# Kernel optimization log

Measured on AMD Instinct MI355X. Metric: run time of the kernel, lower is better.

The kernel has to match this reference:

```python
import jax, jax.numpy as jnp
import numpy as np

B, T, V = 4, 2048, 2048
D = 256   # state_dim
R = 512   # inner_dim
EPS = float(jnp.finfo(jnp.float32).eps)  # F.rms_norm default eps = dtype eps


def rms_norm(x):
    return x * jax.lax.rsqrt(jnp.mean(x * x, axis=-1, keepdims=True) + EPS)


def setup_inputs() -> dict:
    key = jax.random.key(0)
    ks = jax.random.split(key, 9)
    std = 0.02
    return {
        "x": jax.random.normal(ks[0], (B, T, V), dtype=jnp.float32),
        "Wq": jax.random.normal(ks[1], (D, V), dtype=jnp.float32) * std,
        "Wk": jax.random.normal(ks[2], (D, V), dtype=jnp.float32) * std,
        "Wv": jax.random.normal(ks[3], (D, V), dtype=jnp.float32) * std,
        "Wo": jax.random.normal(ks[4], (V, D), dtype=jnp.float32) * std,
        "decay_logit": jnp.float32(3.0),
        "q_out_scale": jnp.float32(0.1),
        "Wdown": jax.random.normal(ks[5], (R, V), dtype=jnp.float32) * std,
        "Wup": jax.random.normal(ks[6], (V, R), dtype=jnp.float32) * std,
        "t_bias": jnp.zeros((R,), dtype=jnp.float32),
        "t_out_scale": jnp.float32(0.1),
        "q_scale": jnp.ones((1,), dtype=jnp.float32),
        "t_scale": jnp.ones((1,), dtype=jnp.float32),
    }


def qtable(x, Wq, Wk, Wv, Wo, decay_logit, out_scale):
    # x: (B,T,V)
    q = jnp.einsum('btv,dv->btd', x, Wq)
    k = jnp.einsum('btv,dv->btd', x, Wk)
    v = jnp.einsum('btv,dv->btd', x, Wv)
    scores = jnp.einsum('btd,bsd->bts', q, k)  # (B,T,T)
    decay = jax.nn.sigmoid(decay_logit)
    pos = jnp.arange(T)
    diff = pos[None, :] - pos[:, None]  # diff[t,s] = s - t ... matches torch (unsqueeze(0)-unsqueeze(1))
    causal = (diff > 0).astype(jnp.float32)
    weights = decay ** jnp.clip(diff.astype(jnp.float32) - 1.0, 0.0, None) * causal
    scores = scores * weights[None, :, :]
    retrieved = jnp.einsum('bts,bsd->btd', scores, v)
    return jnp.einsum('btd,vd->btv', retrieved, Wo) * out_scale


def transform(x, Wdown, Wup, bias, out_scale):
    h = jnp.einsum('btv,rv->btr', x, Wdown) + bias
    h = jax.nn.gelu(h, approximate=False)
    return jnp.einsum('btr,vr->btv', h, Wup) * out_scale


def reference(x, Wq, Wk, Wv, Wo, decay_logit, q_out_scale,
              Wdown, Wup, t_bias, t_out_scale, q_scale, t_scale):
    x = x + q_scale * qtable(rms_norm(x), Wq, Wk, Wv, Wo, decay_logit, q_out_scale)
    x = x + t_scale * transform(rms_norm(x), Wdown, Wup, t_bias, t_out_scale)
    return x
```

## Files before the change

### kernel.cpp

```cpp
#include <hip/hip_runtime.h>
#include <cmath>

typedef _Float16 f16;
typedef _Float16 f16x8 __attribute__((ext_vector_type(8)));
typedef _Float16 f16x4 __attribute__((ext_vector_type(4)));
typedef float f32x4 __attribute__((ext_vector_type(4)));

#define MFMA16(a, b, c) __builtin_amdgcn_mfma_f32_16x16x32_f16(a, b, c, 0, 0, 0)

static constexpr int Bsz = 4;
static constexpr int T = 2048;
static constexpr int V = 2048;
static constexpr int D = 256;
static constexpr int R = 512;
static constexpr int M = Bsz * T;

__device__ __forceinline__ void load_lds16(const f16* g, f16* l) {
    __builtin_amdgcn_global_load_lds(
        (const __attribute__((address_space(1))) unsigned int*)(unsigned long long)g,
        (__attribute__((address_space(3))) unsigned int*)(unsigned int)(unsigned long long)l,
        16, 0, 0);
}

__global__ __launch_bounds__(256) void conv_all(const float* __restrict__ s0,
                                                const float* __restrict__ s1,
                                                const float* __restrict__ s2,
                                                const float* __restrict__ s3,
                                                const float* __restrict__ s4,
                                                const float* __restrict__ s5,
                                                f16* __restrict__ dst) {
    int idx = (blockIdx.x * 256 + threadIdx.x) * 4;
    if (idx >= 4194304) return;
    const float* src; int off;
    if      (idx <  524288) { src = s0; off = idx; }
    else if (idx < 1048576) { src = s1; off = idx - 524288; }
    else if (idx < 1572864) { src = s2; off = idx - 1048576; }
    else if (idx < 2097152) { src = s3; off = idx - 1572864; }
    else if (idx < 3145728) { src = s4; off = idx - 2097152; }
    else                    { src = s5; off = idx - 3145728; }
    float4 v = *(const float4*)&src[off];
    f16x4 o;
    o[0] = (f16)v.x; o[1] = (f16)v.y; o[2] = (f16)v.z; o[3] = (f16)v.w;
    *(f16x4*)&dst[idx] = o;
}

__global__ __launch_bounds__(256) void rmsnorm_kernel(const float* __restrict__ x,
                                                      f16* __restrict__ out) {
    int row = blockIdx.x;
    const float* xr = x + (size_t)row * V;
    int tid = threadIdx.x;
    float4 v0 = ((const float4*)xr)[tid];
    float4 v1 = ((const float4*)xr)[tid + 256];
    float ss = v0.x * v0.x + v0.y * v0.y + v0.z * v0.z + v0.w * v0.w
             + v1.x * v1.x + v1.y * v1.y + v1.z * v1.z + v1.w * v1.w;
    #pragma unroll
    for (int o = 32; o > 0; o >>= 1) ss += __shfl_xor(ss, o);
    __shared__ float wsum[4];
    if ((tid & 63) == 0) wsum[tid >> 6] = ss;
    __syncthreads();
    float tot = wsum[0] + wsum[1] + wsum[2] + wsum[3];
    float s = rsqrtf(tot / (float)V + 1.1920929e-07f);
    f16* orow = out + (size_t)row * V;
    f16x4 o0, o1;
    o0[0] = (f16)(v0.x * s); o0[1] = (f16)(v0.y * s);
    o0[2] = (f16)(v0.z * s); o0[3] = (f16)(v0.w * s);
    o1[0] = (f16)(v1.x * s); o1[1] = (f16)(v1.y * s);
    o1[2] = (f16)(v1.z * s); o1[3] = (f16)(v1.w * s);
    *(f16x4*)&orow[tid * 4] = o0;
    *(f16x4*)&orow[1024 + tid * 4] = o1;
}

__global__ __launch_bounds__(256) void rmsnorm_f16(const f16* __restrict__ x,
                                                   f16* __restrict__ out) {
    int row = blockIdx.x;
    int tid = threadIdx.x;
    const f16* xr = x + (size_t)row * V;
    f16x8 v = *(const f16x8*)&xr[tid * 8];
    float f[8];
    float ss = 0.f;
    #pragma unroll
    for (int j = 0; j < 8; j++) { f[j] = (float)v[j]; ss += f[j] * f[j]; }
    #pragma unroll
    for (int o = 32; o > 0; o >>= 1) ss += __shfl_xor(ss, o);
    __shared__ float wsum[4];
    if ((tid & 63) == 0) wsum[tid >> 6] = ss;
    __syncthreads();
    float tot = wsum[0] + wsum[1] + wsum[2] + wsum[3];
    float s = rsqrtf(tot / (float)V + 1.1920929e-07f);
    f16x8 o;
    #pragma unroll
    for (int j = 0; j < 8; j++) o[j] = (f16)(f[j] * s);
    *(f16x8*)&out[(size_t)row * V + tid * 8] = o;
}

struct GemmEpi {
    const float* residf;
    const f16* residh;
    float* outf;
    f16* outh;
    f16* out_q; f16* out_k; f16* out_vT;
    f16* out_h;
    const float* bias;
    const float* sA; const float* sB;
};

template <int MODE>
__device__ __forceinline__ void epi_store(const GemmEpi& e, float s, f32x4 a,
                                          int gm_base, int gn) {
    #pragma unroll
    for (int i = 0; i < 4; i++) {
        int gm = gm_base + i;
        float vv = a[i];
        if (MODE == 0) {
            if (gn < 256) {
                e.out_q[(size_t)gm * D + gn] = (f16)vv;
            } else if (gn < 512) {
                e.out_k[(size_t)gm * D + (gn - 256)] = (f16)vv;
            } else {
                int d = gn - 512;
                int b = gm >> 11, t = gm & 2047;
                e.out_vT[((size_t)b * D + d) * T + t] = (f16)vv;
            }
        } else if (MODE == 1) {
            size_t o = (size_t)gm * V + gn;
            e.outh[o] = (f16)(e.residf[o] + s * vv);
        } else if (MODE == 2) {
            float z = vv + e.bias[gn];
            float g = 0.5f * z * (1.f + erff(z * 0.70710678118654752f));
            e.out_h[(size_t)gm * R + gn] = (f16)g;
        } else {
            size_t o = (size_t)gm * V + gn;
            e.outf[o] = (float)e.residh[o] + s * vv;
        }
    }
}

template <int MODE>
__global__ __launch_bounds__(256) void gemm_nt(const f16* __restrict__ A,
                                               const f16* __restrict__ Bm,
                                               int K, GemmEpi e) {
    __shared__ f16 Asl[2][128 * 32];
    __shared__ f16 Bsl[2][128 * 32];
    int tid = threadIdx.x;
    int lane = tid & 63, wv = tid >> 6;
    int wm = wv >> 1, wn = wv & 1;
    int quad = lane >> 4, l16 = lane & 15;
    int m0 = blockIdx.x * 128, n0 = blockIdx.y * 128;
    f32x4 acc[4][4] = {};

    int srow = lane >> 2;
    int scg = (lane & 3) ^ ((lane >> 3) & 3);
    const f16* Ag0 = &A[(size_t)(m0 + 16 * wv + srow) * K + scg * 8];
    const f16* Ag1 = &A[(size_t)(m0 + 16 * (wv + 4) + srow) * K + scg * 8];
    const f16* Bg0 = &Bm[(size_t)(n0 + 16 * wv + srow) * K + scg * 8];
    const f16* Bg1 = &Bm[(size_t)(n0 + 16 * (wv + 4) + srow) * K + scg * 8];
    int lo0 = (16 * wv) * 32, lo1 = (16 * (wv + 4)) * 32;

    int fs = quad ^ ((l16 >> 1) & 3);
    int niter = K >> 5;

    load_lds16(Ag0, &Asl[0][lo0]);
    load_lds16(Ag1, &Asl[0][lo1]);
    load_lds16(Bg0, &Bsl[0][lo0]);
    load_lds16(Bg1, &Bsl[0][lo1]);

    for (int i = 0; i < niter; i++) {
        int cur = i & 1;
        __builtin_amdgcn_s_barrier();
        if (i + 1 < niter) {
            int k0 = (i + 1) << 5;
            int nb = cur ^ 1;
            load_lds16(Ag0 + k0, &Asl[nb][lo0]);
            load_lds16(Ag1 + k0, &Asl[nb][lo1]);
            load_lds16(Bg0 + k0, &Bsl[nb][lo0]);
            load_lds16(Bg1 + k0, &Bsl[nb][lo1]);
            asm volatile("s_waitcnt vmcnt(4)" ::: "memory");
        } else {
            asm volatile("s_waitcnt vmcnt(0)" ::: "memory");
        }
        __builtin_amdgcn_s_barrier();
        f16x8 af[4], bf[4];
        #pragma unroll
        for (int j = 0; j < 4; j++)
            af[j] = *(const f16x8*)&Asl[cur][(64 * wm + 16 * j + l16) * 32 + fs * 8];
        #pragma unroll
        for (int j = 0; j < 4; j++)
            bf[j] = *(const f16x8*)&Bsl[cur][(64 * wn + 16 * j + l16) * 32 + fs * 8];
        #pragma unroll
        for (int mi = 0; mi < 4; mi++)
            #pragma unroll
            for (int ni = 0; ni < 4; ni++)
                acc[mi][ni] = MFMA16(af[mi], bf[ni], acc[mi][ni]);
    }

    float s = 0.f;
    if (MODE == 1 || MODE == 3) s = e.sA[0] * e.sB[0];
    #pragma unroll
    for (int mi = 0; mi < 4; mi++)
        #pragma unroll
        for (int ni = 0; ni < 4; ni++)
            epi_store<MODE>(e, s, acc[mi][ni],
                            m0 + 64 * wm + 16 * mi + quad * 4,
                            n0 + 64 * wn + 16 * ni + l16);
}

template <int MODE>
__global__ __launch_bounds__(256) void gemm_nt_k64(const f16* __restrict__ A,
                                                   const f16* __restrict__ Bm,
                                                   int K, GemmEpi e) {
    __shared__ f16 Asl[2][128 * 64];
    __shared__ f16 Bsl[2][128 * 64];
    int tid = threadIdx.x;
    int lane = tid & 63, wv = tid >> 6;
    int wm = wv >> 1, wn = wv & 1;
    int quad = lane >> 4, l16 = lane & 15;
    int m0 = blockIdx.x * 128, n0 = blockIdx.y * 128;
    f32x4 acc[4][4] = {};

    int r8 = lane >> 3;
    int gcol = (lane & 7) ^ r8;
    const f16* Ag[4]; const f16* Bg[4]; int lo[4];
    #pragma unroll
    for (int j = 0; j < 4; j++) {
        int rbase = 8 * (wv + 4 * j);
        Ag[j] = &A[(size_t)(m0 + rbase + r8) * K + gcol * 8];
        Bg[j] = &Bm[(size_t)(n0 + rbase + r8) * K + gcol * 8];
        lo[j] = rbase * 64;
    }
    int niter = K >> 6;

    #pragma unroll
    for (int j = 0; j < 4; j++) {
        load_lds16(Ag[j], &Asl[0][lo[j]]);
        load_lds16(Bg[j], &Bsl[0][lo[j]]);
    }

    for (int i = 0; i < niter; i++) {
        int cur = i & 1;
        __builtin_amdgcn_s_barrier();
        if (i + 1 < niter) {
            int k0 = (i + 1) << 6;
            int nb = cur ^ 1;
            #pragma unroll
            for (int j = 0; j < 4; j++) {
                load_lds16(Ag[j] + k0, &Asl[nb][lo[j]]);
                load_lds16(Bg[j] + k0, &Bsl[nb][lo[j]]);
            }
            asm volatile("s_waitcnt vmcnt(8)" ::: "memory");
        } else {
            asm volatile("s_waitcnt vmcnt(0)" ::: "memory");
        }
        __builtin_amdgcn_s_barrier();
        #pragma unroll
        for (int kk = 0; kk < 2; kk++) {
            f16x8 af[4], bf[4];
            #pragma unroll
            for (int j = 0; j < 4; j++) {
                int row = 64 * wm + 16 * j + l16;
                int sl = (kk * 4 + quad) ^ (l16 & 7);
                af[j] = *(const f16x8*)&Asl[cur][row * 64 + sl * 8];
            }
            #pragma unroll
            for (int j = 0; j < 4; j++) {
                int row = 64 * wn + 16 * j + l16;
                int sl = (kk * 4 + quad) ^ (l16 & 7);
                bf[j] = *(const f16x8*)&Bsl[cur][row * 64 + sl * 8];
            }
            #pragma unroll
            for (int mi = 0; mi < 4; mi++)
                #pragma unroll
                for (int ni = 0; ni < 4; ni++)
                    acc[mi][ni] = MFMA16(af[mi], bf[ni], acc[mi][ni]);
        }
    }

    float s = 0.f;
    if (MODE == 1 || MODE == 3) s = e.sA[0] * e.sB[0];
    #pragma unroll
    for (int mi = 0; mi < 4; mi++)
        #pragma unroll
        for (int ni = 0; ni < 4; ni++)
            epi_store<MODE>(e, s, acc[mi][ni],
                            m0 + 64 * wm + 16 * mi + quad * 4,
                            n0 + 64 * wn + 16 * ni + l16);
}

__global__ __launch_bounds__(256) void attn_kernel(const f16* __restrict__ q,
                                                   const f16* __restrict__ k,
                                                   const f16* __restrict__ vT,
                                                   f16* __restrict__ ret,
                                                   const float* __restrict__ decay_logit) {
    __shared__ f16 Psl[32 * 72];
    int tid = threadIdx.x, lane = tid & 63, wv = tid >> 6;
    int quad = lane >> 4, l16 = lane & 15;
    int b = blockIdx.y, t0 = blockIdx.x * 32;
    const f16* qb = q + (size_t)b * T * D;
    const f16* kb = k + (size_t)b * T * D;
    const f16* vb = vT + (size_t)b * D * T;
    f16* rb = ret + (size_t)b * T * D;

    float dl = decay_logit[0];
    float decay = 1.f / (1.f + expf(-dl));
    float l2d = log2f(decay);
    float nl2d = -l2d;

    f16x8 qf[2][8];
    #pragma unroll
    for (int mi = 0; mi < 2; mi++)
        #pragma unroll
        for (int kk = 0; kk < 8; kk++)
            qf[mi][kk] = *(const f16x8*)&qb[(size_t)(t0 + 16 * mi + l16) * D + kk * 32 + quad * 8];

    f32x4 acc2[2][4] = {};

    for (int s0 = t0; s0 < T; s0 += 64) {
        if ((float)(s0 - t0 - 32) * nl2d > 25.f) break;
        int srow = s0 + 16 * wv + l16;
        int srcl = srow < T ? srow : T - 1;
        f32x4 sacc[2] = {};
        #pragma unroll
        for (int kk = 0; kk < 8; kk++) {
            f16x8 bf = *(const f16x8*)&kb[(size_t)srcl * D + kk * 32 + quad * 8];
            sacc[0] = MFMA16(qf[0][kk], bf, sacc[0]);
            sacc[1] = MFMA16(qf[1][kk], bf, sacc[1]);
        }
        __syncthreads();
        #pragma unroll
        for (int mi = 0; mi < 2; mi++) {
            #pragma unroll
            for (int i = 0; i < 4; i++) {
                int t_ = t0 + 16 * mi + quad * 4 + i;
                int diff = srow - t_;
                float w = (diff > 0 && srow < T) ? exp2f((float)(diff - 1) * l2d) : 0.f;
                Psl[(16 * mi + quad * 4 + i) * 72 + 16 * wv + l16] = (f16)(sacc[mi][i] * w);
            }
        }
        __syncthreads();
        #pragma unroll
        for (int kk = 0; kk < 2; kk++) {
            int sb = s0 + kk * 32 + quad * 8;
            if (sb >= T) sb = T - 8;
            f16x8 pa[2], vf[4];
            #pragma unroll
            for (int mi = 0; mi < 2; mi++)
                pa[mi] = *(const f16x8*)&Psl[(16 * mi + l16) * 72 + kk * 32 + quad * 8];
            #pragma unroll
            for (int ni = 0; ni < 4; ni++)
                vf[ni] = *(const f16x8*)&vb[(size_t)(64 * wv + 16 * ni + l16) * T + sb];
            #pragma unroll
            for (int mi = 0; mi < 2; mi++)
                #pragma unroll
                for (int ni = 0; ni < 4; ni++)
                    acc2[mi][ni] = MFMA16(pa[mi], vf[ni], acc2[mi][ni]);
        }
    }

    #pragma unroll
    for (int mi = 0; mi < 2; mi++) {
        #pragma unroll
        for (int ni = 0; ni < 4; ni++) {
            int t_ = t0 + 16 * mi + quad * 4;
            int d_ = 64 * wv + 16 * ni + l16;
            #pragma unroll
            for (int i = 0; i < 4; i++)
                rb[(size_t)(t_ + i) * D + d_] = (f16)acc2[mi][ni][i];
        }
    }
}

extern "C" void kernel_launch(void* const* d_in, const int* in_sizes, int n_in,
                              void* d_out, int out_size, void* d_ws, size_t ws_size,
                              hipStream_t stream) {
    const float* x           = (const float*)d_in[0];
    const float* Wq          = (const float*)d_in[1];
    const float* Wk          = (const float*)d_in[2];
    const float* Wv          = (const float*)d_in[3];
    const float* Wo          = (const float*)d_in[4];
    const float* decay_logit = (const float*)d_in[5];
    const float* q_out_scale = (const float*)d_in[6];
    const float* Wdown       = (const float*)d_in[7];
    const float* Wup         = (const float*)d_in[8];
    const float* t_bias      = (const float*)d_in[9];
    const float* t_out_scale = (const float*)d_in[10];
    const float* q_scale     = (const float*)d_in[11];
    const float* t_scale     = (const float*)d_in[12];

    char* ws = (char*)d_ws;
    f16* Wqkv16  = (f16*)ws;  ws += (size_t)768 * V * 2;
    f16* Wo16    = (f16*)ws;  ws += (size_t)V * D * 2;
    f16* Wdown16 = (f16*)ws;  ws += (size_t)R * V * 2;
    f16* Wup16   = (f16*)ws;  ws += (size_t)V * R * 2;
    f16* xn16    = (f16*)ws;  ws += (size_t)M * V * 2;
    f16* q16     = (f16*)ws;  ws += (size_t)M * D * 2;
    f16* k16     = (f16*)ws;  ws += (size_t)M * D * 2;
    f16* vT16    = (f16*)ws;  ws += (size_t)Bsz * D * T * 2;
    f16* ret16   = (f16*)ws;  ws += (size_t)M * D * 2;
    f16* x2_16   = (f16*)ws;  ws += (size_t)M * V * 2;
    f16* h16     = q16;

    float* out = (float*)d_out;

    conv_all<<<dim3(4096), 256, 0, stream>>>(Wq, Wk, Wv, Wo, Wdown, Wup, Wqkv16);

    rmsnorm_kernel<<<dim3(M), 256, 0, stream>>>(x, xn16);

    {
        GemmEpi e = {};
        e.out_q = q16; e.out_k = k16; e.out_vT = vT16;
        gemm_nt_k64<0><<<dim3(M / 128, 768 / 128), 256, 0, stream>>>(xn16, Wqkv16, V, e);
    }

    attn_kernel<<<dim3(T / 32, Bsz), 256, 0, stream>>>(q16, k16, vT16, ret16, decay_logit);

    {
        GemmEpi e = {};
        e.residf = x; e.outh = x2_16; e.sA = q_scale; e.sB = q_out_scale;
        gemm_nt<1><<<dim3(M / 128, V / 128), 256, 0, stream>>>(ret16, Wo16, D, e);
    }

    rmsnorm_f16<<<dim3(M), 256, 0, stream>>>(x2_16, xn16);

    {
        GemmEpi e = {};
        e.out_h = h16; e.bias = t_bias;
        gemm_nt_k64<2><<<dim3(M / 128, R / 128), 256, 0, stream>>>(xn16, Wdown16, V, e);
    }

    {
        GemmEpi e = {};
        e.residh = x2_16; e.outf = out; e.sA = t_scale; e.sB = t_out_scale;
        gemm_nt<3><<<dim3(M / 128, V / 128), 256, 0, stream>>>(h16, Wup16, R, e);
    }
}
```

Measured before the change: 318.6 us.

## Rewrite K=2048 GEMMs as 8-wave triple-buffered ping-pong pipeline with priority

The two large-K GEMMs (QKV projection and down projection) now use a 512-thread, 8-wave kernel with a triple-buffered LDS ring that prefetches two tiles ahead. Each wave computes a 32x64 sub-tile, and the A and B prefetches are split across the two k-halves. Barriers and s_setprio bracket the MFMA bursts so one group of waves computes while others load. The aim is to hide global-to-LDS latency and raise MFMA utilisation, at the cost of more LDS (96KB) and lower occupancy per CU.

Result: no change. 321.6 us (+0.9%).

```diff
diff --git a/kernel.cpp b/kernel.cpp
--- a/kernel.cpp
+++ b/kernel.cpp
@@ -205,83 +205,97 @@
 }
 
 template <int MODE>
-__global__ __launch_bounds__(256) void gemm_nt_k64(const f16* __restrict__ A,
-                                                   const f16* __restrict__ Bm,
-                                                   int K, GemmEpi e) {
-    __shared__ f16 Asl[2][128 * 64];
-    __shared__ f16 Bsl[2][128 * 64];
+__global__ __launch_bounds__(512) void gemm_nt_p8(const f16* __restrict__ A,
+                                                  const f16* __restrict__ Bm,
+                                                  int K, GemmEpi e) {
+    __shared__ f16 Asl[3][128 * 64];
+    __shared__ f16 Bsl[3][128 * 64];
     int tid = threadIdx.x;
     int lane = tid & 63, wv = tid >> 6;
     int wm = wv >> 1, wn = wv & 1;
     int quad = lane >> 4, l16 = lane & 15;
     int m0 = blockIdx.x * 128, n0 = blockIdx.y * 128;
-    f32x4 acc[4][4] = {};
+    f32x4 acc[2][4] = {};
 
     int r8 = lane >> 3;
     int gcol = (lane & 7) ^ r8;
-    const f16* Ag[4]; const f16* Bg[4]; int lo[4];
-    #pragma unroll
-    for (int j = 0; j < 4; j++) {
-        int rbase = 8 * (wv + 4 * j);
-        Ag[j] = &A[(size_t)(m0 + rbase + r8) * K + gcol * 8];
-        Bg[j] = &Bm[(size_t)(n0 + rbase + r8) * K + gcol * 8];
-        lo[j] = rbase * 64;
-    }
-    int niter = K >> 6;
-
-    #pragma unroll
-    for (int j = 0; j < 4; j++) {
-        load_lds16(Ag[j], &Asl[0][lo[j]]);
-        load_lds16(Bg[j], &Bsl[0][lo[j]]);
-    }
-
-    for (int i = 0; i < niter; i++) {
-        int cur = i & 1;
-        __builtin_amdgcn_s_barrier();
-        if (i + 1 < niter) {
-            int k0 = (i + 1) << 6;
-            int nb = cur ^ 1;
-            #pragma unroll
-            for (int j = 0; j < 4; j++) {
-                load_lds16(Ag[j] + k0, &Asl[nb][lo[j]]);
-                load_lds16(Bg[j] + k0, &Bsl[nb][lo[j]]);
-            }
-            asm volatile("s_waitcnt vmcnt(8)" ::: "memory");
-        } else {
-            asm volatile("s_waitcnt vmcnt(0)" ::: "memory");
-        }
-        __builtin_amdgcn_s_barrier();
-        #pragma unroll
-        for (int kk = 0; kk < 2; kk++) {
-            f16x8 af[4], bf[4];
-            #pragma unroll
-            for (int j = 0; j < 4; j++) {
-                int row = 64 * wm + 16 * j + l16;
-                int sl = (kk * 4 + quad) ^ (l16 & 7);
-                af[j] = *(const f16x8*)&Asl[cur][row * 64 + sl * 8];
-            }
-            #pragma unroll
-            for (int j = 0; j < 4; j++) {
-                int row = 64 * wn + 16 * j + l16;
-                int sl = (kk * 4 + quad) ^ (l16 & 7);
-                bf[j] = *(const f16x8*)&Bsl[cur][row * 64 + sl * 8];
-            }
-            #pragma unroll
-            for (int mi = 0; mi < 4; mi++)
-                #pragma unroll
-                for (int ni = 0; ni < 4; ni++)
-                    acc[mi][ni] = MFMA16(af[mi], bf[ni], acc[mi][ni]);
-        }
+    const f16* Ag0 = &A [(size_t)(m0 +      8 * wv + r8) * K + gcol * 8];
+    const f16* Ag1 = &A [(size_t)(m0 + 64 + 8 * wv + r8) * K + gcol * 8];
+    const f16* Bg0 = &Bm[(size_t)(n0 +      8 * wv + r8) * K + gcol * 8];
+    const f16* Bg1 = &Bm[(size_t)(n0 + 64 + 8 * wv + r8) * K + gcol * 8];
+    int lo0 = (8 * wv) * 64, lo1 = (64 + 8 * wv) * 64;
+
+    int nt = K >> 6;
+
+    load_lds16(Ag0, &Asl[0][lo0]); load_lds16(Ag1, &Asl[0][lo1]);
+    load_lds16(Bg0, &Bsl[0][lo0]); load_lds16(Bg1, &Bsl[0][lo1]);
+    load_lds16(Ag0 + 64, &Asl[1][lo0]); load_lds16(Ag1 + 64, &Asl[1][lo1]);
+    load_lds16(Bg0 + 64, &Bsl[1][lo0]); load_lds16(Bg1 + 64, &Bsl[1][lo1]);
+    asm volatile("s_waitcnt vmcnt(4)" ::: "memory");
+    __builtin_amdgcn_s_barrier();
+
+    int c0 = 0, c1 = 1, c2 = 2;
+    for (int t = 0; t < nt; t++) {
+        f16* Ac = &Asl[0][0] + c0 * (128 * 64);
+        f16* Bc = &Bsl[0][0] + c0 * (128 * 64);
+        f16* An = &Asl[0][0] + c2 * (128 * 64);
+        f16* Bn = &Bsl[0][0] + c2 * (128 * 64);
+        bool pf = (t + 2 < nt);
+        int k2 = (t + 2) << 6;
+
+        if (pf) { load_lds16(Ag0 + k2, An + lo0); load_lds16(Ag1 + k2, An + lo1); }
+        f16x8 af0[2], bf0[4];
+        {
+            int sl = quad ^ (l16 & 7);
+            af0[0] = *(const f16x8*)&Ac[(32 * wm      + l16) * 64 + sl * 8];
+            af0[1] = *(const f16x8*)&Ac[(32 * wm + 16 + l16) * 64 + sl * 8];
+            #pragma unroll
+            for (int ni = 0; ni < 4; ni++)
+                bf0[ni] = *(const f16x8*)&Bc[(64 * wn + 16 * ni + l16) * 64 + sl * 8];
+        }
+        __builtin_amdgcn_s_barrier();
+        __builtin_amdgcn_s_setprio(1);
+        #pragma unroll
+        for (int mi = 0; mi < 2; mi++)
+            #pragma unroll
+            for (int ni = 0; ni < 4; ni++)
+                acc[mi][ni] = MFMA16(af0[mi], bf0[ni], acc[mi][ni]);
+        __builtin_amdgcn_s_setprio(0);
+        __builtin_amdgcn_s_barrier();
+
+        if (pf) { load_lds16(Bg0 + k2, Bn + lo0); load_lds16(Bg1 + k2, Bn + lo1); }
+        f16x8 af1[2], bf1[4];
+        {
+            int sl = (4 + quad) ^ (l16 & 7);
+            af1[0] = *(const f16x8*)&Ac[(32 * wm      + l16) * 64 + sl * 8];
+            af1[1] = *(const f16x8*)&Ac[(32 * wm + 16 + l16) * 64 + sl * 8];
+            #pragma unroll
+            for (int ni = 0; ni < 4; ni++)
+                bf1[ni] = *(const f16x8*)&Bc[(64 * wn + 16 * ni + l16) * 64 + sl * 8];
+        }
+        if (pf) asm volatile("s_waitcnt vmcnt(4)" ::: "memory");
+        else    asm volatile("s_waitcnt vmcnt(0)" ::: "memory");
+        __builtin_amdgcn_s_barrier();
+        __builtin_amdgcn_s_setprio(1);
+        #pragma unroll
+        for (int mi = 0; mi < 2; mi++)
+            #pragma unroll
+            for (int ni = 0; ni < 4; ni++)
+                acc[mi][ni] = MFMA16(af1[mi], bf1[ni], acc[mi][ni]);
+        __builtin_amdgcn_s_setprio(0);
+        __builtin_amdgcn_s_barrier();
+
+        int tmp = c0; c0 = c1; c1 = c2; c2 = tmp;
     }
 
     float s = 0.f;
     if (MODE == 1 || MODE == 3) s = e.sA[0] * e.sB[0];
     #pragma unroll
-    for (int mi = 0; mi < 4; mi++)
+    for (int mi = 0; mi < 2; mi++)
         #pragma unroll
         for (int ni = 0; ni < 4; ni++)
             epi_store<MODE>(e, s, acc[mi][ni],
-                            m0 + 64 * wm + 16 * mi + quad * 4,
+                            m0 + 32 * wm + 16 * mi + quad * 4,
                             n0 + 64 * wn + 16 * ni + l16);
 }
 
@@ -407,7 +421,7 @@
     {
         GemmEpi e = {};
         e.out_q = q16; e.out_k = k16; e.out_vT = vT16;
-        gemm_nt_k64<0><<<dim3(M / 128, 768 / 128), 256, 0, stream>>>(xn16, Wqkv16, V, e);
+        gemm_nt_p8<0><<<dim3(M / 128, 768 / 128), 512, 0, stream>>>(xn16, Wqkv16, V, e);
     }
 
     attn_kernel<<<dim3(T / 32, Bsz), 256, 0, stream>>>(q16, k16, vT16, ret16, decay_logit);
@@ -423,7 +437,7 @@
     {
         GemmEpi e = {};
         e.out_h = h16; e.bias = t_bias;
-        gemm_nt_k64<2><<<dim3(M / 128, R / 128), 256, 0, stream>>>(xn16, Wdown16, V, e);
+        gemm_nt_p8<2><<<dim3(M / 128, R / 128), 512, 0, stream>>>(xn16, Wdown16, V, e);
     }
 
     {
```

## Use per-wave private LDS tiles in K=2048 GEMMs to drop block barriers

Applied to the files above, without the earlier changes.

Replaces the shared 128x64 double-buffered LDS tiles with per-wave private 64x32 A and B slices. Each wave loads its own rows through global_load_lds, so both s_barrier calls per iteration go away. The cost is that each wave reloads its own copy of data the block used to share: global and L2 traffic for A and B doubles, and the K step halves, which doubles the loop iterations. Removing the barriers may also be unsafe, because without a barrier other lanes' LDS writes may not be visible after a wave-local vmcnt wait.

Result: no change. 323.6 us (+1.6%).

```diff
diff --git a/kernel.cpp b/kernel.cpp
--- a/kernel.cpp
+++ b/kernel.cpp
@@ -205,11 +205,10 @@
 }
 
 template <int MODE>
-__global__ __launch_bounds__(256) void gemm_nt_k64(const f16* __restrict__ A,
-                                                   const f16* __restrict__ Bm,
-                                                   int K, GemmEpi e) {
-    __shared__ f16 Asl[2][128 * 64];
-    __shared__ f16 Bsl[2][128 * 64];
+__global__ __launch_bounds__(256) void gemm_nt_wp(const f16* __restrict__ A,
+                                                  const f16* __restrict__ Bm,
+                                                  int K, GemmEpi e) {
+    __shared__ f16 SL[2][4][2][64 * 32];
     int tid = threadIdx.x;
     int lane = tid & 63, wv = tid >> 6;
     int wm = wv >> 1, wn = wv & 1;
@@ -217,61 +216,49 @@
     int m0 = blockIdx.x * 128, n0 = blockIdx.y * 128;
     f32x4 acc[4][4] = {};
 
-    int r8 = lane >> 3;
-    int gcol = (lane & 7) ^ r8;
-    const f16* Ag[4]; const f16* Bg[4]; int lo[4];
+    int srow = lane >> 2;
+    int scg = (lane & 3) ^ ((lane >> 3) & 3);
+    const f16* Ag[4]; const f16* Bg[4];
     #pragma unroll
     for (int j = 0; j < 4; j++) {
-        int rbase = 8 * (wv + 4 * j);
-        Ag[j] = &A[(size_t)(m0 + rbase + r8) * K + gcol * 8];
-        Bg[j] = &Bm[(size_t)(n0 + rbase + r8) * K + gcol * 8];
-        lo[j] = rbase * 64;
-    }
-    int niter = K >> 6;
+        Ag[j] = &A [(size_t)(m0 + 64 * wm + 16 * j + srow) * K + scg * 8];
+        Bg[j] = &Bm[(size_t)(n0 + 64 * wn + 16 * j + srow) * K + scg * 8];
+    }
+
+    int fs = quad ^ ((l16 >> 1) & 3);
+    int niter = K >> 5;
 
     #pragma unroll
     for (int j = 0; j < 4; j++) {
-        load_lds16(Ag[j], &Asl[0][lo[j]]);
-        load_lds16(Bg[j], &Bsl[0][lo[j]]);
+        load_lds16(Ag[j], &SL[0][wv][0][16 * j * 32]);
+        load_lds16(Bg[j], &SL[0][wv][1][16 * j * 32]);
     }
 
     for (int i = 0; i < niter; i++) {
         int cur = i & 1;
-        __builtin_amdgcn_s_barrier();
         if (i + 1 < niter) {
-            int k0 = (i + 1) << 6;
+            int k0 = (i + 1) << 5;
             int nb = cur ^ 1;
             #pragma unroll
             for (int j = 0; j < 4; j++) {
-                load_lds16(Ag[j] + k0, &Asl[nb][lo[j]]);
-                load_lds16(Bg[j] + k0, &Bsl[nb][lo[j]]);
+                load_lds16(Ag[j] + k0, &SL[nb][wv][0][16 * j * 32]);
+                load_lds16(Bg[j] + k0, &SL[nb][wv][1][16 * j * 32]);
             }
             asm volatile("s_waitcnt vmcnt(8)" ::: "memory");
         } else {
             asm volatile("s_waitcnt vmcnt(0)" ::: "memory");
         }
-        __builtin_amdgcn_s_barrier();
-        #pragma unroll
-        for (int kk = 0; kk < 2; kk++) {
-            f16x8 af[4], bf[4];
-            #pragma unroll
-            for (int j = 0; j < 4; j++) {
-                int row = 64 * wm + 16 * j + l16;
-                int sl = (kk * 4 + quad) ^ (l16 & 7);
-                af[j] = *(const f16x8*)&Asl[cur][row * 64 + sl * 8];
-            }
-            #pragma unroll
-            for (int j = 0; j < 4; j++) {
-                int row = 64 * wn + 16 * j + l16;
-                int sl = (kk * 4 + quad) ^ (l16 & 7);
-                bf[j] = *(const f16x8*)&Bsl[cur][row * 64 + sl * 8];
-            }
-            #pragma unroll
-            for (int mi = 0; mi < 4; mi++)
-                #pragma unroll
-                for (int ni = 0; ni < 4; ni++)
-                    acc[mi][ni] = MFMA16(af[mi], bf[ni], acc[mi][ni]);
-        }
+        f16x8 af[4], bf[4];
+        #pragma unroll
+        for (int j = 0; j < 4; j++) {
+            af[j] = *(const f16x8*)&SL[cur][wv][0][(16 * j + l16) * 32 + fs * 8];
+            bf[j] = *(const f16x8*)&SL[cur][wv][1][(16 * j + l16) * 32 + fs * 8];
+        }
+        #pragma unroll
+        for (int mi = 0; mi < 4; mi++)
+            #pragma unroll
+            for (int ni = 0; ni < 4; ni++)
+                acc[mi][ni] = MFMA16(af[mi], bf[ni], acc[mi][ni]);
     }
 
     float s = 0.f;
@@ -407,7 +394,7 @@
     {
         GemmEpi e = {};
         e.out_q = q16; e.out_k = k16; e.out_vT = vT16;
-        gemm_nt_k64<0><<<dim3(M / 128, 768 / 128), 256, 0, stream>>>(xn16, Wqkv16, V, e);
+        gemm_nt_wp<0><<<dim3(M / 128, 768 / 128), 256, 0, stream>>>(xn16, Wqkv16, V, e);
     }
 
     attn_kernel<<<dim3(T / 32, Bsz), 256, 0, stream>>>(q16, k16, vT16, ret16, decay_logit);
@@ -423,7 +410,7 @@
     {
         GemmEpi e = {};
         e.out_h = h16; e.bias = t_bias;
-        gemm_nt_k64<2><<<dim3(M / 128, R / 128), 256, 0, stream>>>(xn16, Wdown16, V, e);
+        gemm_nt_wp<2><<<dim3(M / 128, R / 128), 256, 0, stream>>>(xn16, Wdown16, V, e);
     }
 
     {
```

## Fuse second RMSNorm into Wo GEMM epilogue and Wdown GEMM scaling

Applied to the files above, without the earlier changes.

Drops the standalone f16 RMSNorm pass. The Wo GEMM epilogue now accumulates per-row sums of squares of the new residual, reducing them through LDS and adding them into a global buffer with atomics. The Wdown GEMM reads the unnormalized f16 residual and applies the per-row rsqrt scale in its epilogue before the bias and GELU. This saves one full read and write of the M×V activation and one launch, at the cost of atomics, a memset, and a small precision change from feeding unnormalized values to the GEMM.

Result: faster. 306.1 us (-3.9%).

```diff
diff --git a/kernel.cpp b/kernel.cpp
--- a/kernel.cpp
+++ b/kernel.cpp
@@ -70,29 +70,6 @@
     *(f16x4*)&orow[1024 + tid * 4] = o1;
 }
 
-__global__ __launch_bounds__(256) void rmsnorm_f16(const f16* __restrict__ x,
-                                                   f16* __restrict__ out) {
-    int row = blockIdx.x;
-    int tid = threadIdx.x;
-    const f16* xr = x + (size_t)row * V;
-    f16x8 v = *(const f16x8*)&xr[tid * 8];
-    float f[8];
-    float ss = 0.f;
-    #pragma unroll
-    for (int j = 0; j < 8; j++) { f[j] = (float)v[j]; ss += f[j] * f[j]; }
-    #pragma unroll
-    for (int o = 32; o > 0; o >>= 1) ss += __shfl_xor(ss, o);
-    __shared__ float wsum[4];
-    if ((tid & 63) == 0) wsum[tid >> 6] = ss;
-    __syncthreads();
-    float tot = wsum[0] + wsum[1] + wsum[2] + wsum[3];
-    float s = rsqrtf(tot / (float)V + 1.1920929e-07f);
-    f16x8 o;
-    #pragma unroll
-    for (int j = 0; j < 8; j++) o[j] = (f16)(f[j] * s);
-    *(f16x8*)&out[(size_t)row * V + tid * 8] = o;
-}
-
 struct GemmEpi {
     const float* residf;
     const f16* residh;
@@ -102,6 +79,7 @@
     f16* out_h;
     const float* bias;
     const float* sA; const float* sB;
+    float* rowss;
 };
 
 template <int MODE>
@@ -125,7 +103,8 @@
             size_t o = (size_t)gm * V + gn;
             e.outh[o] = (f16)(e.residf[o] + s * vv);
         } else if (MODE == 2) {
-            float z = vv + e.bias[gn];
+            float sc = rsqrtf(e.rowss[gm] * (1.f / 2048.f) + 1.1920929e-07f);
+            float z = sc * vv + e.bias[gn];
             float g = 0.5f * z * (1.f + erff(z * 0.70710678118654752f));
             e.out_h[(size_t)gm * R + gn] = (f16)g;
         } else {
@@ -195,13 +174,44 @@
 
     float s = 0.f;
     if (MODE == 1 || MODE == 3) s = e.sA[0] * e.sB[0];
-    #pragma unroll
-    for (int mi = 0; mi < 4; mi++)
-        #pragma unroll
-        for (int ni = 0; ni < 4; ni++)
-            epi_store<MODE>(e, s, acc[mi][ni],
-                            m0 + 64 * wm + 16 * mi + quad * 4,
-                            n0 + 64 * wn + 16 * ni + l16);
+
+    if constexpr (MODE == 1) {
+        float* rbuf = (float*)&Asl[0][0];
+        __syncthreads();
+        #pragma unroll
+        for (int mi = 0; mi < 4; mi++) {
+            #pragma unroll
+            for (int i = 0; i < 4; i++) {
+                int rl = 64 * wm + 16 * mi + quad * 4 + i;
+                int gm = m0 + rl;
+                float p = 0.f;
+                #pragma unroll
+                for (int ni = 0; ni < 4; ni++) {
+                    int gn = n0 + 64 * wn + 16 * ni + l16;
+                    size_t o = (size_t)gm * V + gn;
+                    float val = e.residf[o] + s * acc[mi][ni][i];
+                    e.outh[o] = (f16)val;
+                    p += val * val;
+                }
+                rbuf[rl * 32 + wn * 16 + l16] = p;
+            }
+        }
+        __syncthreads();
+        if (tid < 128) {
+            float tot = 0.f;
+            #pragma unroll
+            for (int j = 0; j < 32; j++) tot += rbuf[tid * 32 + j];
+            atomicAdd(&e.rowss[m0 + tid], tot);
+        }
+    } else {
+        #pragma unroll
+        for (int mi = 0; mi < 4; mi++)
+            #pragma unroll
+            for (int ni = 0; ni < 4; ni++)
+                epi_store<MODE>(e, s, acc[mi][ni],
+                                m0 + 64 * wm + 16 * mi + quad * 4,
+                                n0 + 64 * wn + 16 * ni + l16);
+    }
 }
 
 template <int MODE>
@@ -396,11 +406,13 @@
     f16* vT16    = (f16*)ws;  ws += (size_t)Bsz * D * T * 2;
     f16* ret16   = (f16*)ws;  ws += (size_t)M * D * 2;
     f16* x2_16   = (f16*)ws;  ws += (size_t)M * V * 2;
+    float* rowss = (float*)ws; ws += (size_t)M * 4;
     f16* h16     = q16;
 
     float* out = (float*)d_out;
 
     conv_all<<<dim3(4096), 256, 0, stream>>>(Wq, Wk, Wv, Wo, Wdown, Wup, Wqkv16);
+    hipMemsetAsync(rowss, 0, (size_t)M * 4, stream);
 
     rmsnorm_kernel<<<dim3(M), 256, 0, stream>>>(x, xn16);
 
@@ -415,15 +427,15 @@
     {
         GemmEpi e = {};
         e.residf = x; e.outh = x2_16; e.sA = q_scale; e.sB = q_out_scale;
+        e.rowss = rowss;
         gemm_nt<1><<<dim3(M / 128, V / 128), 256, 0, stream>>>(ret16, Wo16, D, e);
     }
 
-    rmsnorm_f16<<<dim3(M), 256, 0, stream>>>(x2_16, xn16);
 
     {
         GemmEpi e = {};
-        e.out_h = h16; e.bias = t_bias;
-        gemm_nt_k64<2><<<dim3(M / 128, R / 128), 256, 0, stream>>>(xn16, Wdown16, V, e);
+        e.out_h = h16; e.bias = t_bias; e.rowss = rowss;
+        gemm_nt_k64<2><<<dim3(M / 128, R / 128), 256, 0, stream>>>(x2_16, Wdown16, V, e);
     }
 
     {
```
